# Kernel optimization log

Hardware: AMD Instinct MI355X
Metric: run time of the kernel (lower is better)

## Reference

```python
import jax, jax.numpy as jnp
import numpy as np

N_NODES = 50000
N_EDGES = 1600000
DIM = 512


def setup_inputs() -> dict:
    key = jax.random.key(0)
    k1, k2, k3, k4, k5 = jax.random.split(key, 5)
    x = jax.random.normal(k1, (N_NODES, DIM), dtype=jnp.float32)
    adj_rows = jax.random.randint(k2, (N_EDGES,), 0, N_NODES, dtype=jnp.int32)
    adj_cols = jax.random.randint(k3, (N_EDGES,), 0, N_NODES, dtype=jnp.int32)
    adj_vals = jax.random.uniform(k4, (N_EDGES,), dtype=jnp.float32)
    # fc1 weight [out_dim, in_dim], kaiming-normal-ish init
    weight = jax.random.normal(k5, (DIM, DIM), dtype=jnp.float32) * np.float32(np.sqrt(2.0 / DIM))
    scale = jnp.full((1,), 1.5, dtype=jnp.float32)
    return {"x": x, "adj_rows": adj_rows, "adj_cols": adj_cols,
            "adj_vals": adj_vals, "weight": weight, "scale": scale}


def reference(x, adj_rows, adj_cols, adj_vals, weight, scale):
    # dropout in eval mode -> identity
    N, D = x.shape
    # dense linear: y = x @ W^T
    y = jnp.einsum('nd,od->no', x, weight)
    # sparse adj @ y  (COO SpMM via gather + segment_sum)
    y = jax.ops.segment_sum(adj_vals[:, None] * y[adj_cols], adj_rows,
                            num_segments=N)
    # sp_norm: mean-center over nodes, scale by global RMS^{-1} * (1+scale) * sqrt(D)
    y_t = y - jnp.mean(y, axis=0, keepdims=True)
    y_norm = jnp.mean(jnp.sum(y_t * y_t, axis=1)) ** -0.5
    y = y_t * y_norm * (1.0 + scale) * jnp.float32(np.sqrt(D))
    # activation (relu), then residual (input_dim == output_dim)
    y = jax.nn.relu(y)
    return y + x
```

## Files before the change

### kernel.cpp

```cpp
#include <hip/hip_runtime.h>
#include <hip/hip_bf16.h>
#include <cstdint>
#include <cstddef>

#define N_NODES 50000
#define DIM 512
#define N_EDGES 1600000
#define NT 25
#define NB (N_NODES * NT)

typedef __bf16 bf16;
typedef __bf16 bf16x8 __attribute__((ext_vector_type(8)));
typedef __bf16 bf16x4 __attribute__((ext_vector_type(4)));
typedef float floatx4 __attribute__((ext_vector_type(4)));

__global__ void cast_kernel(const float* __restrict__ in, bf16* __restrict__ out, int n4) {
    int i = blockIdx.x * blockDim.x + threadIdx.x;
    if (i >= n4) return;
    float4 v = reinterpret_cast<const float4*>(in)[i];
    bf16x4 o;
    o[0] = (bf16)v.x; o[1] = (bf16)v.y; o[2] = (bf16)v.z; o[3] = (bf16)v.w;
    reinterpret_cast<bf16x4*>(out)[i] = o;
}

__global__ void hist_kernel(const int* __restrict__ rows, const int* __restrict__ cols,
                            int* __restrict__ cnt, int E) {
    int i = blockIdx.x * blockDim.x + threadIdx.x;
    if (i < E) {
        int key = rows[i] * NT + (cols[i] >> 11);
        atomicAdd(&cnt[key], 1);
    }
}

__global__ __launch_bounds__(1024) void scanA_kernel(const int* __restrict__ cnt,
                                                     int* __restrict__ row_start,
                                                     int* __restrict__ blksum, int n) {
    __shared__ int s[1024];
    const int t = threadIdx.x;
    int i = blockIdx.x * 1024 + t;
    int v = (i < n) ? cnt[i] : 0;
    s[t] = v;
    __syncthreads();
    for (int off = 1; off < 1024; off <<= 1) {
        int u = (t >= off) ? s[t - off] : 0;
        __syncthreads();
        s[t] += u;
        __syncthreads();
    }
    if (i < n) row_start[i] = s[t] - v;
    if (t == 1023) blksum[blockIdx.x] = s[1023];
}

__global__ __launch_bounds__(1024) void scanB_kernel(const int* __restrict__ blksum,
                                                     int* __restrict__ blkoff, int nb) {
    __shared__ int s[1024];
    const int t = threadIdx.x;
    const int base = t * 2;
    int a = (base < nb) ? blksum[base] : 0;
    int b = (base + 1 < nb) ? blksum[base + 1] : 0;
    s[t] = a + b;
    __syncthreads();
    for (int off = 1; off < 1024; off <<= 1) {
        int u = (t >= off) ? s[t - off] : 0;
        __syncthreads();
        s[t] += u;
        __syncthreads();
    }
    int excl = (t == 0) ? 0 : s[t - 1];
    if (base < nb) blkoff[base] = excl;
    if (base + 1 < nb) blkoff[base + 1] = excl + a;
}

__global__ __launch_bounds__(1024) void scanC_kernel(int* __restrict__ row_start,
                                                     const int* __restrict__ blkoff,
                                                     int* __restrict__ cursor, int n) {
    int i = blockIdx.x * 1024 + threadIdx.x;
    if (i >= n) return;
    int v = row_start[i] + blkoff[i >> 10];
    row_start[i] = v;
    cursor[i] = v;
    if (i == n - 1) row_start[n] = N_EDGES;
}

__global__ void scatter_kernel(const int* __restrict__ rows, const int* __restrict__ cols,
                               const float* __restrict__ vals, int* __restrict__ cursor,
                               int2* __restrict__ ecv, int E) {
    int i = blockIdx.x * blockDim.x + threadIdx.x;
    if (i >= E) return;
    int c = cols[i];
    int key = rows[i] * NT + (c >> 11);
    int p = atomicAdd(&cursor[key], 1);
    ecv[p] = make_int2(c, __float_as_int(vals[i]));
}

__global__ __launch_bounds__(256) void gemm_kernel(const bf16* __restrict__ A,
                                                   const bf16* __restrict__ B,
                                                   bf16* __restrict__ C) {
    __shared__ bf16 lA[128 * 32];
    __shared__ bf16 lB[128 * 32];
    const int t = threadIdx.x;
    const int wave = t >> 6;
    const int lane = t & 63;
    const int rowBase = blockIdx.x * 128;
    const int colBase = blockIdx.y * 128;
    const int wm = (wave >> 1) * 64;
    const int wn = (wave & 1) * 64;
    floatx4 acc[4][4] = {};

    const int r_a = t >> 2;
    const int kk = (t & 3) * 8;

    const int l15 = lane & 15;
    const int koff = (lane >> 4) * 8;

    for (int k0 = 0; k0 < DIM; k0 += 32) {
#pragma unroll
        for (int j = 0; j < 2; j++) {
            int row = rowBase + r_a + j * 64;
            if (row > N_NODES - 1) row = N_NODES - 1;
            const bf16* g = A + (size_t)row * DIM + k0 + kk;
            bf16* l = lA + wave * 512 + j * 2048;
            __builtin_amdgcn_global_load_lds(
                (const __attribute__((address_space(1))) void*)g,
                (__attribute__((address_space(3))) void*)l, 16, 0, 0);
        }
#pragma unroll
        for (int j = 0; j < 2; j++) {
            int row = colBase + r_a + j * 64;
            const bf16* g = B + (size_t)row * DIM + k0 + kk;
            bf16* l = lB + wave * 512 + j * 2048;
            __builtin_amdgcn_global_load_lds(
                (const __attribute__((address_space(1))) void*)g,
                (__attribute__((address_space(3))) void*)l, 16, 0, 0);
        }
        __syncthreads();
        bf16x8 af[4], bfr[4];
#pragma unroll
        for (int i = 0; i < 4; i++)
            af[i] = *reinterpret_cast<const bf16x8*>(lA + (wm + i * 16 + l15) * 32 + koff);
#pragma unroll
        for (int j = 0; j < 4; j++)
            bfr[j] = *reinterpret_cast<const bf16x8*>(lB + (wn + j * 16 + l15) * 32 + koff);
#pragma unroll
        for (int i = 0; i < 4; i++)
#pragma unroll
            for (int j = 0; j < 4; j++)
                acc[i][j] = __builtin_amdgcn_mfma_f32_16x16x32_bf16(af[i], bfr[j], acc[i][j], 0, 0, 0);
        __syncthreads();
    }
    const int rquad = (lane >> 4) * 4;
#pragma unroll
    for (int i = 0; i < 4; i++) {
#pragma unroll
        for (int reg = 0; reg < 4; reg++) {
            int gr = rowBase + wm + i * 16 + rquad + reg;
            if (gr >= N_NODES) continue;
#pragma unroll
            for (int j = 0; j < 4; j++) {
                int gc = colBase + wn + j * 16 + l15;
                C[(size_t)gr * DIM + gc] = (bf16)acc[i][j][reg];
            }
        }
    }
}

__device__ __forceinline__ float blo(uint32_t w) { return __uint_as_float(w << 16); }
__device__ __forceinline__ float bhi(uint32_t w) { return __uint_as_float(w & 0xffff0000u); }

__device__ __forceinline__ void fmac8(float* acc, float v, const uint4& w) {
    acc[0] += v * blo(w.x); acc[1] += v * bhi(w.x);
    acc[2] += v * blo(w.y); acc[3] += v * bhi(w.y);
    acc[4] += v * blo(w.z); acc[5] += v * bhi(w.z);
    acc[6] += v * blo(w.w); acc[7] += v * bhi(w.w);
}

__device__ __forceinline__ uint4 grow(const uint32_t* yb, int col, int lane) {
    return *reinterpret_cast<const uint4*>(yb + (size_t)col * 256 + lane * 4);
}

__global__ __launch_bounds__(256) void spmm_kernel(const int* __restrict__ row_start,
                                                   const int2* __restrict__ ecv,
                                                   const bf16* __restrict__ y,
                                                   float* __restrict__ y2) {
    const int wave = threadIdx.x >> 6;
    const int lane = threadIdx.x & 63;
    const int r = blockIdx.x * 4 + wave;
    const int s = row_start[r * NT];
    const int e = row_start[(r + 1) * NT];
    float acc[8] = {0.f, 0.f, 0.f, 0.f, 0.f, 0.f, 0.f, 0.f};
    const uint32_t* yb = reinterpret_cast<const uint32_t*>(y);

    int i = s;
    if ((i & 1) && i < e) {
        int2 e0 = ecv[i];
        uint4 w0 = grow(yb, e0.x, lane);
        fmac8(acc, __int_as_float(e0.y), w0);
        i++;
    }
    for (; i + 8 <= e; i += 8) {
        const int4* p = reinterpret_cast<const int4*>(ecv + i);
        int4 p0 = p[0], p1 = p[1], p2 = p[2], p3 = p[3];
        uint4 w0 = grow(yb, p0.x, lane);
        uint4 w1 = grow(yb, p0.z, lane);
        uint4 w2 = grow(yb, p1.x, lane);
        uint4 w3 = grow(yb, p1.z, lane);
        uint4 w4 = grow(yb, p2.x, lane);
        uint4 w5 = grow(yb, p2.z, lane);
        uint4 w6 = grow(yb, p3.x, lane);
        uint4 w7 = grow(yb, p3.z, lane);
        fmac8(acc, __int_as_float(p0.y), w0);
        fmac8(acc, __int_as_float(p0.w), w1);
        fmac8(acc, __int_as_float(p1.y), w2);
        fmac8(acc, __int_as_float(p1.w), w3);
        fmac8(acc, __int_as_float(p2.y), w4);
        fmac8(acc, __int_as_float(p2.w), w5);
        fmac8(acc, __int_as_float(p3.y), w6);
        fmac8(acc, __int_as_float(p3.w), w7);
    }
    for (; i + 2 <= e; i += 2) {
        int4 p0 = *reinterpret_cast<const int4*>(ecv + i);
        uint4 w0 = grow(yb, p0.x, lane);
        uint4 w1 = grow(yb, p0.z, lane);
        fmac8(acc, __int_as_float(p0.y), w0);
        fmac8(acc, __int_as_float(p0.w), w1);
    }
    if (i < e) {
        int2 e0 = ecv[i];
        uint4 w0 = grow(yb, e0.x, lane);
        fmac8(acc, __int_as_float(e0.y), w0);
    }
    float4* out = reinterpret_cast<float4*>(y2 + (size_t)r * DIM + lane * 8);
    out[0] = make_float4(acc[0], acc[1], acc[2], acc[3]);
    out[1] = make_float4(acc[4], acc[5], acc[6], acc[7]);
}

#define RED_GRID 512
__global__ __launch_bounds__(256) void reduce_kernel(const float* __restrict__ y2,
                                                     float* __restrict__ colsum,
                                                     float* __restrict__ totsq) {
    const int t = threadIdx.x;
    const int d2 = t * 2;
    float c0 = 0.f, c1 = 0.f, sq = 0.f;
    for (int r = blockIdx.x; r < N_NODES; r += RED_GRID * 2) {
        float2 v = *reinterpret_cast<const float2*>(y2 + (size_t)r * DIM + d2);
        int r2 = r + RED_GRID;
        float2 u = (r2 < N_NODES)
                       ? *reinterpret_cast<const float2*>(y2 + (size_t)r2 * DIM + d2)
                       : make_float2(0.f, 0.f);
        c0 += v.x + u.x;
        c1 += v.y + u.y;
        sq += v.x * v.x + v.y * v.y + u.x * u.x + u.y * u.y;
    }
    atomicAdd(&colsum[d2], c0);
    atomicAdd(&colsum[d2 + 1], c1);
    __shared__ float ssq[256];
    ssq[t] = sq;
    __syncthreads();
    for (int off = 128; off > 0; off >>= 1) {
        if (t < off) ssq[t] += ssq[t + off];
        __syncthreads();
    }
    if (t == 0) atomicAdd(totsq, ssq[0]);
}

__global__ void scalar_kernel(const float* __restrict__ colsum, const float* __restrict__ totsq,
                              const float* __restrict__ scale, float* __restrict__ sfac) {
    __shared__ float sm[512];
    const int t = threadIdx.x;
    float mu = colsum[t] * (1.0f / N_NODES);
    sm[t] = mu * mu;
    __syncthreads();
    for (int off = 256; off > 0; off >>= 1) {
        if (t < off) sm[t] += sm[t + off];
        __syncthreads();
    }
    if (t == 0) {
        float var = totsq[0] * (1.0f / N_NODES) - sm[0];
        sfac[0] = rsqrtf(var) * (1.0f + scale[0]) * sqrtf((float)DIM);
    }
}

__global__ void final_kernel(float* __restrict__ y2, const float* __restrict__ x,
                             const float* __restrict__ colsum, const float* __restrict__ sfac,
                             int n4) {
    int i = blockIdx.x * blockDim.x + threadIdx.x;
    if (i >= n4) return;
    const float invN = 1.0f / N_NODES;
    float4 v = reinterpret_cast<float4*>(y2)[i];
    float4 xv = reinterpret_cast<const float4*>(x)[i];
    float4 mu = reinterpret_cast<const float4*>(colsum)[i & 127];
    float s = sfac[0];
    v.x = fmaxf((v.x - mu.x * invN) * s, 0.0f) + xv.x;
    v.y = fmaxf((v.y - mu.y * invN) * s, 0.0f) + xv.y;
    v.z = fmaxf((v.z - mu.z * invN) * s, 0.0f) + xv.z;
    v.w = fmaxf((v.w - mu.w * invN) * s, 0.0f) + xv.w;
    reinterpret_cast<float4*>(y2)[i] = v;
}

extern "C" void kernel_launch(void* const* d_in, const int* in_sizes, int n_in,
                              void* d_out, int out_size, void* d_ws, size_t ws_size,
                              hipStream_t stream) {
    const float* x        = (const float*)d_in[0];
    const int*   adj_rows = (const int*)d_in[1];
    const int*   adj_cols = (const int*)d_in[2];
    const float* adj_vals = (const float*)d_in[3];
    const float* weight   = (const float*)d_in[4];
    const float* scale    = (const float*)d_in[5];
    float* out = (float*)d_out;

    char* ws = (char*)d_ws;
    size_t off = 0;
    auto alloc = [&](size_t b) {
        char* p = ws + off;
        off += (b + 255) & ~(size_t)255;
        return p;
    };
    const int nblk = (NB + 1023) / 1024;
    bf16*  xb        = (bf16*)alloc((size_t)N_NODES * DIM * 2);
    int2*  ecv       = (int2*)xb;
    bf16*  Wb        = (bf16*)alloc((size_t)DIM * DIM * 2);
    bf16*  y         = (bf16*)alloc((size_t)N_NODES * DIM * 2);
    int*   cnt       = (int*)alloc((size_t)NB * 4);
    int*   cursor    = cnt;
    int*   row_start = (int*)alloc((size_t)(NB + 1) * 4);
    int*   blksum    = (int*)alloc((size_t)nblk * 4);
    int*   blkoff    = (int*)alloc((size_t)nblk * 4);
    float* colsum    = (float*)alloc(512 * 4);
    float* totsq     = (float*)alloc(4);
    float* sfac      = (float*)alloc(4);
    (void)ws_size; (void)in_sizes; (void)n_in; (void)out_size;

    hipMemsetAsync(cnt, 0, (size_t)NB * 4, stream);
    hipMemsetAsync(colsum, 0, 512 * 4, stream);
    hipMemsetAsync(totsq, 0, 4, stream);

    const int n4x = N_NODES * DIM / 4;
    const int n4w = DIM * DIM / 4;
    cast_kernel<<<(n4x + 255) / 256, 256, 0, stream>>>(x, xb, n4x);
    cast_kernel<<<(n4w + 255) / 256, 256, 0, stream>>>(weight, Wb, n4w);

    gemm_kernel<<<dim3((N_NODES + 127) / 128, DIM / 128), 256, 0, stream>>>(xb, Wb, y);

    hist_kernel<<<(N_EDGES + 255) / 256, 256, 0, stream>>>(adj_rows, adj_cols, cnt, N_EDGES);
    scanA_kernel<<<nblk, 1024, 0, stream>>>(cnt, row_start, blksum, NB);
    scanB_kernel<<<1, 1024, 0, stream>>>(blksum, blkoff, nblk);
    scanC_kernel<<<nblk, 1024, 0, stream>>>(row_start, blkoff, cursor, NB);
    scatter_kernel<<<(N_EDGES + 255) / 256, 256, 0, stream>>>(adj_rows, adj_cols, adj_vals,
                                                              cursor, ecv, N_EDGES);

    spmm_kernel<<<N_NODES / 4, 256, 0, stream>>>(row_start, ecv, y, out);

    reduce_kernel<<<RED_GRID, 256, 0, stream>>>(out, colsum, totsq);
    scalar_kernel<<<1, 512, 0, stream>>>(colsum, totsq, scale, sfac);
    final_kernel<<<(n4x + 255) / 256, 256, 0, stream>>>(out, x, colsum, sfac, n4x);
}
```

Measured before the change: 715.2 us.

## Fuse column-sum/RMS reduction into SpMM and software-pipeline the edge gather loop

The SpMM kernel now accumulates per-column sums and the total sum of squares into 64 shadow buffers via atomics, and the separate reduce kernel is removed. This avoids re-reading the 100MB output. The edge loop is double-buffered so the next batch of edge descriptors is loaded while the current gathers are in flight, with nontemporal loads and stores. It also adds launch_bounds occupancy hints. The cost is many atomics per wave (8 per lane plus one) and higher register pressure.

```diff
diff --git a/kernel.cpp b/kernel.cpp
--- a/kernel.cpp
+++ b/kernel.cpp
@@ -8,11 +8,13 @@
 #define N_EDGES 1600000
 #define NT 25
 #define NB (N_NODES * NT)
+#define NSHADOW 64
 
 typedef __bf16 bf16;
 typedef __bf16 bf16x8 __attribute__((ext_vector_type(8)));
 typedef __bf16 bf16x4 __attribute__((ext_vector_type(4)));
 typedef float floatx4 __attribute__((ext_vector_type(4)));
+typedef int intx4 __attribute__((ext_vector_type(4)));
 
 __global__ void cast_kernel(const float* __restrict__ in, bf16* __restrict__ out, int n4) {
     int i = blockIdx.x * blockDim.x + threadIdx.x;
@@ -178,45 +180,102 @@
     return *reinterpret_cast<const uint4*>(yb + (size_t)col * 256 + lane * 4);
 }
 
-__global__ __launch_bounds__(256) void spmm_kernel(const int* __restrict__ row_start,
-                                                   const int2* __restrict__ ecv,
-                                                   const bf16* __restrict__ y,
-                                                   float* __restrict__ y2) {
+#define LOADD(d0, d1, d2, d3, base)                                      \
+    do {                                                                 \
+        const intx4* p_ = reinterpret_cast<const intx4*>(ecv + (base));  \
+        d0 = __builtin_nontemporal_load(p_);                             \
+        d1 = __builtin_nontemporal_load(p_ + 1);                         \
+        d2 = __builtin_nontemporal_load(p_ + 2);                         \
+        d3 = __builtin_nontemporal_load(p_ + 3);                         \
+    } while (0)
+
+#define GATHER8(g, d0, d1, d2, d3)          \
+    do {                                    \
+        g##0 = grow(yb, d0.x, lane);        \
+        g##1 = grow(yb, d0.z, lane);        \
+        g##2 = grow(yb, d1.x, lane);        \
+        g##3 = grow(yb, d1.z, lane);        \
+        g##4 = grow(yb, d2.x, lane);        \
+        g##5 = grow(yb, d2.z, lane);        \
+        g##6 = grow(yb, d3.x, lane);        \
+        g##7 = grow(yb, d3.z, lane);        \
+    } while (0)
+
+#define EXTRACTV(v, d0, d1, d2, d3)         \
+    do {                                    \
+        v##0 = __int_as_float(d0.y);        \
+        v##1 = __int_as_float(d0.w);        \
+        v##2 = __int_as_float(d1.y);        \
+        v##3 = __int_as_float(d1.w);        \
+        v##4 = __int_as_float(d2.y);        \
+        v##5 = __int_as_float(d2.w);        \
+        v##6 = __int_as_float(d3.y);        \
+        v##7 = __int_as_float(d3.w);        \
+    } while (0)
+
+#define FMAC8X8(g, v)                       \
+    do {                                    \
+        fmac8(acc, v##0, g##0);             \
+        fmac8(acc, v##1, g##1);             \
+        fmac8(acc, v##2, g##2);             \
+        fmac8(acc, v##3, g##3);             \
+        fmac8(acc, v##4, g##4);             \
+        fmac8(acc, v##5, g##5);             \
+        fmac8(acc, v##6, g##6);             \
+        fmac8(acc, v##7, g##7);             \
+    } while (0)
+
+__global__ __launch_bounds__(256, 3) void spmm_kernel(const int* __restrict__ row_start,
+                                                      const int2* __restrict__ ecv,
+                                                      const bf16* __restrict__ y,
+                                                      float* __restrict__ y2,
+                                                      float* __restrict__ colsumS,
+                                                      float* __restrict__ totsqS) {
     const int wave = threadIdx.x >> 6;
     const int lane = threadIdx.x & 63;
     const int r = blockIdx.x * 4 + wave;
-    const int s = row_start[r * NT];
+    int i = row_start[r * NT];
     const int e = row_start[(r + 1) * NT];
     float acc[8] = {0.f, 0.f, 0.f, 0.f, 0.f, 0.f, 0.f, 0.f};
     const uint32_t* yb = reinterpret_cast<const uint32_t*>(y);
 
-    int i = s;
     if ((i & 1) && i < e) {
         int2 e0 = ecv[i];
         uint4 w0 = grow(yb, e0.x, lane);
         fmac8(acc, __int_as_float(e0.y), w0);
         i++;
     }
-    for (; i + 8 <= e; i += 8) {
-        const int4* p = reinterpret_cast<const int4*>(ecv + i);
-        int4 p0 = p[0], p1 = p[1], p2 = p[2], p3 = p[3];
-        uint4 w0 = grow(yb, p0.x, lane);
-        uint4 w1 = grow(yb, p0.z, lane);
-        uint4 w2 = grow(yb, p1.x, lane);
-        uint4 w3 = grow(yb, p1.z, lane);
-        uint4 w4 = grow(yb, p2.x, lane);
-        uint4 w5 = grow(yb, p2.z, lane);
-        uint4 w6 = grow(yb, p3.x, lane);
-        uint4 w7 = grow(yb, p3.z, lane);
-        fmac8(acc, __int_as_float(p0.y), w0);
-        fmac8(acc, __int_as_float(p0.w), w1);
-        fmac8(acc, __int_as_float(p1.y), w2);
-        fmac8(acc, __int_as_float(p1.w), w3);
-        fmac8(acc, __int_as_float(p2.y), w4);
-        fmac8(acc, __int_as_float(p2.w), w5);
-        fmac8(acc, __int_as_float(p3.y), w6);
-        fmac8(acc, __int_as_float(p3.w), w7);
-    }
+    int nb = (e - i) >> 3;
+
+    if (nb >= 2) {
+        intx4 A0, A1, A2, A3, B0, B1, B2, B3;
+        uint4 gA0, gA1, gA2, gA3, gA4, gA5, gA6, gA7;
+        uint4 gB0, gB1, gB2, gB3, gB4, gB5, gB6, gB7;
+        float vA0, vA1, vA2, vA3, vA4, vA5, vA6, vA7;
+        float vB0, vB1, vB2, vB3, vB4, vB5, vB6, vB7;
+
+        LOADD(A0, A1, A2, A3, i);
+        LOADD(B0, B1, B2, B3, i + 8);
+        EXTRACTV(vA, A0, A1, A2, A3);
+        GATHER8(gA, A0, A1, A2, A3);
+        int k = 1;
+        while (true) {
+            EXTRACTV(vB, B0, B1, B2, B3);
+            if (k + 1 < nb) LOADD(A0, A1, A2, A3, i + (k + 1) * 8);
+            GATHER8(gB, B0, B1, B2, B3);
+            FMAC8X8(gA, vA);
+            k++;
+            if (k >= nb) { FMAC8X8(gB, vB); break; }
+            EXTRACTV(vA, A0, A1, A2, A3);
+            if (k + 1 < nb) LOADD(B0, B1, B2, B3, i + (k + 1) * 8);
+            GATHER8(gA, A0, A1, A2, A3);
+            FMAC8X8(gB, vB);
+            k++;
+            if (k >= nb) { FMAC8X8(gA, vA); break; }
+        }
+        i += nb * 8;
+    }
+
     for (; i + 2 <= e; i += 2) {
         int4 p0 = *reinterpret_cast<const int4*>(ecv + i);
         uint4 w0 = grow(yb, p0.x, lane);
@@ -229,54 +288,49 @@
         uint4 w0 = grow(yb, e0.x, lane);
         fmac8(acc, __int_as_float(e0.y), w0);
     }
-    float4* out = reinterpret_cast<float4*>(y2 + (size_t)r * DIM + lane * 8);
-    out[0] = make_float4(acc[0], acc[1], acc[2], acc[3]);
-    out[1] = make_float4(acc[4], acc[5], acc[6], acc[7]);
-}
-
-#define RED_GRID 512
-__global__ __launch_bounds__(256) void reduce_kernel(const float* __restrict__ y2,
-                                                     float* __restrict__ colsum,
-                                                     float* __restrict__ totsq) {
-    const int t = threadIdx.x;
-    const int d2 = t * 2;
-    float c0 = 0.f, c1 = 0.f, sq = 0.f;
-    for (int r = blockIdx.x; r < N_NODES; r += RED_GRID * 2) {
-        float2 v = *reinterpret_cast<const float2*>(y2 + (size_t)r * DIM + d2);
-        int r2 = r + RED_GRID;
-        float2 u = (r2 < N_NODES)
-                       ? *reinterpret_cast<const float2*>(y2 + (size_t)r2 * DIM + d2)
-                       : make_float2(0.f, 0.f);
-        c0 += v.x + u.x;
-        c1 += v.y + u.y;
-        sq += v.x * v.x + v.y * v.y + u.x * u.x + u.y * u.y;
-    }
-    atomicAdd(&colsum[d2], c0);
-    atomicAdd(&colsum[d2 + 1], c1);
-    __shared__ float ssq[256];
-    ssq[t] = sq;
-    __syncthreads();
-    for (int off = 128; off > 0; off >>= 1) {
-        if (t < off) ssq[t] += ssq[t + off];
-        __syncthreads();
-    }
-    if (t == 0) atomicAdd(totsq, ssq[0]);
-}
-
-__global__ void scalar_kernel(const float* __restrict__ colsum, const float* __restrict__ totsq,
-                              const float* __restrict__ scale, float* __restrict__ sfac) {
+
+    floatx4* out = reinterpret_cast<floatx4*>(y2 + (size_t)r * DIM + lane * 8);
+    floatx4 o0 = {acc[0], acc[1], acc[2], acc[3]};
+    floatx4 o1 = {acc[4], acc[5], acc[6], acc[7]};
+    __builtin_nontemporal_store(o0, out);
+    __builtin_nontemporal_store(o1, out + 1);
+
+    float sq = 0.f;
+#pragma unroll
+    for (int j = 0; j < 8; j++) sq += acc[j] * acc[j];
+#pragma unroll
+    for (int off = 32; off > 0; off >>= 1) sq += __shfl_xor(sq, off, 64);
+    const int sh = (blockIdx.x & (NSHADOW - 1));
+    if (lane == 0) atomicAdd(&totsqS[sh], sq);
+    float* cs = colsumS + sh * DIM + lane * 8;
+#pragma unroll
+    for (int j = 0; j < 8; j++) atomicAdd(&cs[j], acc[j]);
+}
+
+__global__ void scalar_kernel(const float* __restrict__ colsumS, const float* __restrict__ totsqS,
+                              const float* __restrict__ scale, float* __restrict__ sfac,
+                              float* __restrict__ colsum) {
     __shared__ float sm[512];
     const int t = threadIdx.x;
-    float mu = colsum[t] * (1.0f / N_NODES);
+    float s = 0.f;
+#pragma unroll 8
+    for (int c = 0; c < NSHADOW; c++) s += colsumS[c * DIM + t];
+    colsum[t] = s;
+    float mu = s * (1.0f / N_NODES);
     sm[t] = mu * mu;
     __syncthreads();
     for (int off = 256; off > 0; off >>= 1) {
         if (t < off) sm[t] += sm[t + off];
         __syncthreads();
     }
-    if (t == 0) {
-        float var = totsq[0] * (1.0f / N_NODES) - sm[0];
-        sfac[0] = rsqrtf(var) * (1.0f + scale[0]) * sqrtf((float)DIM);
+    if (t < 64) {
+        float tq = totsqS[t];
+#pragma unroll
+        for (int off = 32; off > 0; off >>= 1) tq += __shfl_xor(tq, off, 64);
+        if (t == 0) {
+            float var = tq * (1.0f / N_NODES) - sm[0];
+            sfac[0] = rsqrtf(var) * (1.0f + scale[0]) * sqrtf((float)DIM);
+        }
     }
 }
 
@@ -325,14 +379,14 @@
     int*   row_start = (int*)alloc((size_t)(NB + 1) * 4);
     int*   blksum    = (int*)alloc((size_t)nblk * 4);
     int*   blkoff    = (int*)alloc((size_t)nblk * 4);
+    float* colsumS   = (float*)alloc((size_t)NSHADOW * DIM * 4);
+    float* totsqS    = (float*)alloc((size_t)NSHADOW * 4);
     float* colsum    = (float*)alloc(512 * 4);
-    float* totsq     = (float*)alloc(4);
     float* sfac      = (float*)alloc(4);
     (void)ws_size; (void)in_sizes; (void)n_in; (void)out_size;
 
     hipMemsetAsync(cnt, 0, (size_t)NB * 4, stream);
-    hipMemsetAsync(colsum, 0, 512 * 4, stream);
-    hipMemsetAsync(totsq, 0, 4, stream);
+    hipMemsetAsync(colsumS, 0, (size_t)NSHADOW * DIM * 4 + (size_t)NSHADOW * 4 + 256, stream);
 
     const int n4x = N_NODES * DIM / 4;
     const int n4w = DIM * DIM / 4;
@@ -348,9 +402,8 @@
     scatter_kernel<<<(N_EDGES + 255) / 256, 256, 0, stream>>>(adj_rows, adj_cols, adj_vals,
                                                               cursor, ecv, N_EDGES);
 
-    spmm_kernel<<<N_NODES / 4, 256, 0, stream>>>(row_start, ecv, y, out);
-
-    reduce_kernel<<<RED_GRID, 256, 0, stream>>>(out, colsum, totsq);
-    scalar_kernel<<<1, 512, 0, stream>>>(colsum, totsq, scale, sfac);
+    spmm_kernel<<<N_NODES / 4, 256, 0, stream>>>(row_start, ecv, y, out, colsumS, totsqS);
+
+    scalar_kernel<<<1, 512, 0, stream>>>(colsumS, totsqS, scale, sfac, colsum);
     final_kernel<<<(n4x + 255) / 256, 256, 0, stream>>>(out, x, colsum, sfac, n4x);
 }
```

Result: slower. 1.436 ms (+100.8%).
